# Kernel tuning notes

Measured on AMD Instinct MI355X. Metric: run time of the kernel, lower is better.

The kernel has to match this reference:

```python
import jax, jax.numpy as jnp
import numpy as np

NUM_CLASSES = 21
ALPHA = 1.0
NEG_POS_RATIO = 3.0
NEG_FOR_HARD = 100.0
B, N = 128, 8732


def setup_inputs() -> dict:
    key = jax.random.key(0)
    k1, k2, k3, k4, k5 = jax.random.split(key, 5)
    loc_pred = jax.random.normal(k1, (B, N, 4), jnp.float32)
    conf_pred = jax.random.normal(k2, (B, N, NUM_CLASSES), jnp.float32)
    # y_true = [loc_targets(4) | one-hot class(NUM_CLASSES) | pos_indicator(1)]
    loc_t = jax.random.normal(k3, (B, N, 4), jnp.float32)
    pos = (jax.random.uniform(k4, (B, N)) < 0.02).astype(jnp.float32)
    labels = jax.random.randint(k5, (B, N), 1, NUM_CLASSES)
    labels = jnp.where(pos > 0, labels, 0)  # negatives -> background class 0
    onehot = jax.nn.one_hot(labels, NUM_CLASSES, dtype=jnp.float32)
    y_true = jnp.concatenate([loc_t, onehot, pos[..., None]], axis=-1)
    return {"y_true": y_true, "loc_pred": loc_pred, "conf_pred": conf_pred}


def reference(y_true, loc_pred, conf_pred):
    num_boxes = y_true.shape[1]
    # conf part of y_pred is softmaxed before the loss (as in the torch code)
    conf = jax.nn.softmax(conf_pred, axis=-1)                    # (B, N, C)
    # cross-entropy with clamp(1e-7) + log, summed over classes
    conf_loss = -jnp.sum(y_true[:, :, 4:-1] * jnp.log(jnp.clip(conf, 1e-7, None)), axis=-1)  # (B, N)
    # smooth-L1 on the 4 loc coords
    d = y_true[:, :, :4] - loc_pred
    ad = jnp.abs(d)
    loc_loss = jnp.sum(jnp.where(ad < 1.0, 0.5 * d * d, ad - 0.5), axis=-1)  # (B, N)

    pos = y_true[:, :, -1]                                       # (B, N)
    pos_loc_loss = jnp.sum(loc_loss * pos, axis=1)               # (B,)
    pos_conf_loss = jnp.sum(conf_loss * pos, axis=1)             # (B,)

    num_pos = jnp.sum(pos, axis=-1)                              # (B,)
    num_neg = jnp.minimum(NEG_POS_RATIO * num_pos, num_boxes - num_pos)
    has_pos = jnp.sum((num_pos > 0).astype(jnp.float32)) > 0
    num_neg_batch = jnp.where(has_pos, jnp.sum(num_neg), jnp.float32(NEG_FOR_HARD))
    k_neg = jnp.floor(num_neg_batch)  # matches int() truncation in torch

    # hard-negative mining: max non-background confidence on negative anchors
    # confs_start=5, confs_end=4+NUM_CLASSES -> softmax classes 1..NUM_CLASSES-1
    max_confs = ((1.0 - pos) * jnp.sum(conf[:, :, 1:NUM_CLASSES], axis=2)).reshape(-1)  # (B*N,)
    order = jnp.argsort(-max_confs)                              # descending, static shape
    sorted_conf_loss = conf_loss.reshape(-1)[order]
    ranks = jnp.arange(max_confs.shape[0], dtype=jnp.float32)
    neg_conf_loss = jnp.sum(jnp.where(ranks < k_neg, sorted_conf_loss, 0.0))

    num_pos_c = jnp.where(num_pos != 0, num_pos, jnp.ones_like(num_pos))
    total = jnp.sum(pos_conf_loss) + neg_conf_loss + ALPHA * jnp.sum(pos_loc_loss)
    return total / jnp.sum(num_pos_c)
```

## Files before the change

### kernel.cpp

```cpp
#include <hip/hip_runtime.h>

#define BATCH 128
#define NBOX 8732
#define NC 21
#define M (BATCH * NBOX)
#define EBLK 2048
#define SUBB 16
#define CHUNK 546
#define NREP 32
#define CLIP_MAX 16.118095651f

struct Ctl {
  float pos_conf_sum, pos_loc_sum, s_gt, denom;
  unsigned int k_rem, d1, d2, pad;
};

#define OFF_NPP 1024
#define OFF_PCP (OFF_NPP + 8192)
#define OFF_PLP (OFF_PCP + 8192)
#define OFF_REP 32768
#define REPSZ   (NREP * 2048 * 4)
#define OFF_MC  (OFF_REP + 6 * REPSZ)
#define OFF_CL  (OFF_MC + M * 4)
#define ZERO_BYTES OFF_MC

__device__ __forceinline__ unsigned long long mckey(float mc) {
  unsigned long long K = (unsigned long long)((double)mc * 8589934592.0);
  return (K > 0x1FFFFFFFFull) ? 0x1FFFFFFFFull : K;
}

__global__ __launch_bounds__(256) void k_elem(
    const float* __restrict__ yt, const float* __restrict__ lp,
    const float* __restrict__ cp, float* __restrict__ MC,
    float* __restrict__ CL, float* __restrict__ np_part,
    float* __restrict__ pc_part, float* __restrict__ pl_part,
    unsigned int* __restrict__ rep1c, float* __restrict__ rep1s) {
  __shared__ unsigned int hc[2048];
  __shared__ float hs[2048];
  __shared__ float sred[12];
  const int tid = threadIdx.x;
  const int bid = blockIdx.x;
  for (int i = tid; i < 2048; i += 256) { hc[i] = 0u; hs[i] = 0.f; }
  __syncthreads();

  const int batch = bid >> 4;
  const int sub = bid & 15;
  const int base = batch * NBOX + sub * CHUNK;
  const int cnt = (sub == SUBB - 1) ? (NBOX - (SUBB - 1) * CHUNK) : CHUNK;

  float tpc = 0.f, tpl = 0.f, tnp = 0.f;
  for (int i = tid; i < cnt; i += 256) {
    const int e = base + i;
    const float* crow = cp + (size_t)e * NC;
    float cv[NC];
#pragma unroll
    for (int j = 0; j < NC; ++j) cv[j] = crow[j];
    const float2* y2 = (const float2*)(yt + (size_t)e * 26);
    float2 yw[13];
#pragma unroll
    for (int j = 0; j < 13; ++j) yw[j] = y2[j];
    const float4 lv = ((const float4*)lp)[e];
    const float pos = yw[12].y;

    const float d0 = yw[0].x - lv.x, d1 = yw[0].y - lv.y;
    const float d2 = yw[1].x - lv.z, d3 = yw[1].y - lv.w;
    const float a0 = fabsf(d0), a1 = fabsf(d1), a2 = fabsf(d2), a3 = fabsf(d3);
    float ll = ((a0 < 1.f) ? 0.5f * d0 * d0 : a0 - 0.5f)
             + ((a1 < 1.f) ? 0.5f * d1 * d1 : a1 - 0.5f)
             + ((a2 < 1.f) ? 0.5f * d2 * d2 : a2 - 0.5f)
             + ((a3 < 1.f) ? 0.5f * d3 * d3 : a3 - 0.5f);

    float mx = cv[0];
#pragma unroll
    for (int j = 1; j < NC; ++j) mx = fmaxf(mx, cv[j]);
    float plogit = 0.f;
#pragma unroll
    for (int j = 0; j < NC; ++j) {
      const int w = 4 + j;
      const float oh = (w & 1) ? yw[w >> 1].y : yw[w >> 1].x;
      plogit = fmaf(oh, cv[j], plogit);
    }
    float ssum = 0.f, e0 = 0.f;
#pragma unroll
    for (int j = 0; j < NC; ++j) {
      const float ee = __expf(cv[j] - mx);
      ssum += ee;
      if (j == 0) e0 = ee;
    }
    const float cl = fminf(mx + __logf(ssum) - plogit, CLIP_MAX);
    const float mc = (1.f - pos) * ((ssum - e0) / ssum);

    MC[e] = mc;
    CL[e] = cl;
    const unsigned int b1 = (unsigned int)(mckey(mc) >> 22);
    atomicAdd(&hc[b1], 1u);
    atomicAdd(&hs[b1], cl);
    tpc += pos * cl;
    tpl += pos * ll;
    tnp += pos;
  }

#pragma unroll
  for (int off = 32; off > 0; off >>= 1) {
    tpc += __shfl_down(tpc, off);
    tpl += __shfl_down(tpl, off);
    tnp += __shfl_down(tnp, off);
  }
  if ((tid & 63) == 0) {
    const int w = tid >> 6;
    sred[w] = tpc; sred[4 + w] = tpl; sred[8 + w] = tnp;
  }
  __syncthreads();
  if (tid == 0) {
    pc_part[bid] = sred[0] + sred[1] + sred[2] + sred[3];
    pl_part[bid] = sred[4] + sred[5] + sred[6] + sred[7];
    np_part[bid] = sred[8] + sred[9] + sred[10] + sred[11];
  }
  unsigned int* rc = rep1c + (bid & (NREP - 1)) * 2048;
  float* rs = rep1s + (bid & (NREP - 1)) * 2048;
  for (int i = tid; i < 2048; i += 256)
    if (hc[i]) { atomicAdd(&rc[i], hc[i]); atomicAdd(&rs[i], hs[i]); }
}

template <int LEVEL>
__global__ __launch_bounds__(256) void k_hist(
    const float* __restrict__ MC, const float* __restrict__ CL,
    unsigned int* __restrict__ repc, float* __restrict__ reps,
    const Ctl* __restrict__ ctl) {
  __shared__ unsigned int hc[2048];
  __shared__ float hs[2048];
  for (int i = threadIdx.x; i < 2048; i += 256) { hc[i] = 0u; hs[i] = 0.f; }
  __syncthreads();
  const unsigned int dd = (LEVEL == 2) ? ctl->d1 : ((ctl->d1 << 11) | ctl->d2);
  const float4* M4 = (const float4*)MC;
  const int n4 = M / 4;
  const int stride = gridDim.x * 256;
  for (int i = blockIdx.x * 256 + threadIdx.x; i < n4; i += stride) {
    const float4 m = M4[i];
    const float mv[4] = {m.x, m.y, m.z, m.w};
#pragma unroll
    for (int q = 0; q < 4; ++q) {
      const unsigned long long K = mckey(mv[q]);
      bool match; unsigned int bin;
      if (LEVEL == 2) { match = (unsigned int)(K >> 22) == dd; bin = (unsigned int)(K >> 11) & 2047u; }
      else            { match = (unsigned int)(K >> 11) == dd; bin = (unsigned int)K & 2047u; }
      if (match) {
        const float cl = CL[4 * i + q];
        atomicAdd(&hc[bin], 1u);
        atomicAdd(&hs[bin], cl);
      }
    }
  }
  __syncthreads();
  unsigned int* rc = repc + (blockIdx.x & (NREP - 1)) * 2048;
  float* rs = reps + (blockIdx.x & (NREP - 1)) * 2048;
  for (int i = threadIdx.x; i < 2048; i += 256)
    if (hc[i]) { atomicAdd(&rc[i], hc[i]); atomicAdd(&rs[i], hs[i]); }
}

template <int LEVEL>
__global__ __launch_bounds__(1024) void k_scan(
    const unsigned int* __restrict__ repc, const float* __restrict__ reps,
    const float* __restrict__ np_part, const float* __restrict__ pc_part,
    const float* __restrict__ pl_part, Ctl* __restrict__ ctl,
    float* __restrict__ out) {
  __shared__ unsigned int s[2048];
  __shared__ float sf[2048];
  __shared__ float red[16], rn[16], rh[16], rc[16], ra[16], rb[16];
  __shared__ unsigned int kk;
  __shared__ int win;
  const int tid = threadIdx.x;

  unsigned int c0 = 0, c1 = 0;
  float f0 = 0.f, f1 = 0.f;
  for (int r = 0; r < NREP; ++r) {
    c0 += repc[r * 2048 + tid];
    c1 += repc[r * 2048 + tid + 1024];
    f0 += reps[r * 2048 + tid];
    f1 += reps[r * 2048 + tid + 1024];
  }
  s[tid] = c0; s[tid + 1024] = c1;
  sf[tid] = f0; sf[tid + 1024] = f1;

  if (LEVEL == 1) {
    float np = 0.f;
    if (tid < BATCH)
      for (int j = 0; j < SUBB; ++j) np += np_part[tid * SUBB + j];
    float nn  = fminf(3.0f * np, (float)NBOX - np);
    float hp  = (np > 0.f) ? 1.f : 0.f;
    float npc = (tid < BATCH) ? ((np != 0.f) ? np : 1.f) : 0.f;
    float a = pc_part[tid] + pc_part[tid + 1024];
    float b = pl_part[tid] + pl_part[tid + 1024];
#pragma unroll
    for (int off = 32; off > 0; off >>= 1) {
      nn += __shfl_down(nn, off);   hp += __shfl_down(hp, off);
      npc += __shfl_down(npc, off); a += __shfl_down(a, off);
      b += __shfl_down(b, off);
    }
    const int w = tid >> 6;
    if ((tid & 63) == 0) { rn[w] = nn; rh[w] = hp; rc[w] = npc; ra[w] = a; rb[w] = b; }
    __syncthreads();
    if (tid == 0) {
      float tn = 0.f, th = 0.f, tc = 0.f, ta = 0.f, tb = 0.f;
      for (int i = 0; i < 16; ++i) { tn += rn[i]; th += rh[i]; tc += rc[i]; ta += ra[i]; tb += rb[i]; }
      ctl->denom = tc;
      ctl->pos_conf_sum = ta;
      ctl->pos_loc_sum = tb;
      kk = (unsigned int)floorf((th > 0.f) ? tn : 100.0f);
    }
  } else {
    if (tid == 0) kk = ctl->k_rem;
  }
  if (tid == 0) win = -1;
  __syncthreads();

  const unsigned int krem = kk;
  if (krem != 0) {
    for (int off = 1; off < 2048; off <<= 1) {
      const unsigned int v0 = (tid + off < 2048) ? s[tid + off] : 0u;
      const unsigned int v1 = (tid + 1024 + off < 2048) ? s[tid + 1024 + off] : 0u;
      __syncthreads();
      s[tid] += v0;
      s[tid + 1024] += v1;
      __syncthreads();
    }
#pragma unroll
    for (int t = 0; t < 2; ++t) {
      const int i = tid + t * 1024;
      const unsigned int si = s[i];
      const unsigned int sn = (i < 2047) ? s[i + 1] : 0u;
      if (si >= krem && sn < krem) win = i;
    }
    __syncthreads();
    const int b = win;
    float acc = 0.f;
    if (b >= 0) {
      if (tid > b) acc += sf[tid];
      if (tid + 1024 > b) acc += sf[tid + 1024];
    }
#pragma unroll
    for (int off = 32; off > 0; off >>= 1) acc += __shfl_down(acc, off);
    if ((tid & 63) == 0) red[tid >> 6] = acc;
    __syncthreads();
    if (tid == 0 && b >= 0) {
      float tot = 0.f;
      for (int i = 0; i < 16; ++i) tot += red[i];
      const unsigned int above = (b < 2047) ? s[b + 1] : 0u;
      const unsigned int krem2 = krem - above;
      if (LEVEL < 3) {
        ctl->s_gt += tot;
        ctl->k_rem = krem2;
        if (LEVEL == 1) ctl->d1 = (unsigned int)b;
        else            ctl->d2 = (unsigned int)b;
      } else {
        const unsigned int neq = s[b] - above;
        const float tie = (neq > 0) ? sf[b] * ((float)krem2 / (float)neq) : 0.f;
        const float neg = ctl->s_gt + tot + tie;
        out[0] = (ctl->pos_conf_sum + neg + ctl->pos_loc_sum) / ctl->denom;
      }
    }
  } else if (LEVEL == 3 && tid == 0) {
    out[0] = (ctl->pos_conf_sum + ctl->s_gt + ctl->pos_loc_sum) / ctl->denom;
  }
}

extern "C" void kernel_launch(void* const* d_in, const int* in_sizes, int n_in,
                              void* d_out, int out_size, void* d_ws, size_t ws_size,
                              hipStream_t stream) {
  const float* yt = (const float*)d_in[0];
  const float* lp = (const float*)d_in[1];
  const float* cp = (const float*)d_in[2];
  float* out = (float*)d_out;

  char* ws = (char*)d_ws;
  Ctl* ctl = (Ctl*)ws;
  float* np_part = (float*)(ws + OFF_NPP);
  float* pc_part = (float*)(ws + OFF_PCP);
  float* pl_part = (float*)(ws + OFF_PLP);
  unsigned int* rep1c = (unsigned int*)(ws + OFF_REP);
  float*        rep1s = (float*)(ws + OFF_REP + 1 * REPSZ);
  unsigned int* rep2c = (unsigned int*)(ws + OFF_REP + 2 * REPSZ);
  float*        rep2s = (float*)(ws + OFF_REP + 3 * REPSZ);
  unsigned int* rep3c = (unsigned int*)(ws + OFF_REP + 4 * REPSZ);
  float*        rep3s = (float*)(ws + OFF_REP + 5 * REPSZ);
  float* MC = (float*)(ws + OFF_MC);
  float* CL = (float*)(ws + OFF_CL);

  hipMemsetAsync(ws, 0, ZERO_BYTES, stream);
  k_elem<<<EBLK, 256, 0, stream>>>(yt, lp, cp, MC, CL, np_part, pc_part, pl_part,
                                   rep1c, rep1s);
  k_scan<1><<<1, 1024, 0, stream>>>(rep1c, rep1s, np_part, pc_part, pl_part, ctl, out);
  k_hist<2><<<1024, 256, 0, stream>>>(MC, CL, rep2c, rep2s, ctl);
  k_scan<2><<<1, 1024, 0, stream>>>(rep2c, rep2s, np_part, pc_part, pl_part, ctl, out);
  k_hist<3><<<1024, 256, 0, stream>>>(MC, CL, rep3c, rep3s, ctl);
  k_scan<3><<<1, 1024, 0, stream>>>(rep3c, rep3s, np_part, pc_part, pl_part, ctl, out);
}
```

Before: 289.7 us.

## Process each anchor row with a 32-lane group for coalesced loads; shrink replica histograms

The element kernel now assigns one anchor row to a 32-lane sub-group. Each lane loads one class logit, one y_true entry and one loc coordinate, and max, sum-exp, picked logit and smooth-L1 are combined with shuffle reductions. Before, one thread read a whole 21/26-float row, which gave strided, uncoalesced global loads. The level-2 and level-3 histogram replicas drop from 32 to 8, which shrinks the memset and the scan reads. The per-row work now costs many more shuffles and leaves lanes idle (11 of 32 unused for logits), and there are more global atomic collisions on fewer replicas.

```diff
diff --git a/kernel.cpp b/kernel.cpp
--- a/kernel.cpp
+++ b/kernel.cpp
@@ -7,7 +7,8 @@
 #define EBLK 2048
 #define SUBB 16
 #define CHUNK 546
-#define NREP 32
+#define NREP1 32
+#define NREP2 8
 #define CLIP_MAX 16.118095651f
 
 struct Ctl {
@@ -15,14 +16,21 @@
   unsigned int k_rem, d1, d2, pad;
 };
 
-#define OFF_NPP 1024
+#define OFF_REP 1024
+#define R1SZ    (NREP1 * 2048 * 4)
+#define R23SZ   (NREP2 * 2048 * 4)
+#define OFF_R1C (OFF_REP)
+#define OFF_R1S (OFF_R1C + R1SZ)
+#define OFF_R2C (OFF_R1S + R1SZ)
+#define OFF_R2S (OFF_R2C + R23SZ)
+#define OFF_R3C (OFF_R2S + R23SZ)
+#define OFF_R3S (OFF_R3C + R23SZ)
+#define OFF_NPP (OFF_R3S + R23SZ)
 #define OFF_PCP (OFF_NPP + 8192)
 #define OFF_PLP (OFF_PCP + 8192)
-#define OFF_REP 32768
-#define REPSZ   (NREP * 2048 * 4)
-#define OFF_MC  (OFF_REP + 6 * REPSZ)
+#define OFF_MC  (OFF_PLP + 8192)
 #define OFF_CL  (OFF_MC + M * 4)
-#define ZERO_BYTES OFF_MC
+#define ZERO_BYTES OFF_NPP
 
 __device__ __forceinline__ unsigned long long mckey(float mc) {
   unsigned long long K = (unsigned long long)((double)mc * 8589934592.0);
@@ -47,57 +55,54 @@
   const int sub = bid & 15;
   const int base = batch * NBOX + sub * CHUNK;
   const int cnt = (sub == SUBB - 1) ? (NBOX - (SUBB - 1) * CHUNK) : CHUNK;
+  const int g = tid >> 5;
+  const int j = tid & 31;
 
   float tpc = 0.f, tpl = 0.f, tnp = 0.f;
-  for (int i = tid; i < cnt; i += 256) {
-    const int e = base + i;
-    const float* crow = cp + (size_t)e * NC;
-    float cv[NC];
-#pragma unroll
-    for (int j = 0; j < NC; ++j) cv[j] = crow[j];
-    const float2* y2 = (const float2*)(yt + (size_t)e * 26);
-    float2 yw[13];
-#pragma unroll
-    for (int j = 0; j < 13; ++j) yw[j] = y2[j];
-    const float4 lv = ((const float4*)lp)[e];
-    const float pos = yw[12].y;
-
-    const float d0 = yw[0].x - lv.x, d1 = yw[0].y - lv.y;
-    const float d2 = yw[1].x - lv.z, d3 = yw[1].y - lv.w;
-    const float a0 = fabsf(d0), a1 = fabsf(d1), a2 = fabsf(d2), a3 = fabsf(d3);
-    float ll = ((a0 < 1.f) ? 0.5f * d0 * d0 : a0 - 0.5f)
-             + ((a1 < 1.f) ? 0.5f * d1 * d1 : a1 - 0.5f)
-             + ((a2 < 1.f) ? 0.5f * d2 * d2 : a2 - 0.5f)
-             + ((a3 < 1.f) ? 0.5f * d3 * d3 : a3 - 0.5f);
-
-    float mx = cv[0];
-#pragma unroll
-    for (int j = 1; j < NC; ++j) mx = fmaxf(mx, cv[j]);
-    float plogit = 0.f;
-#pragma unroll
-    for (int j = 0; j < NC; ++j) {
-      const int w = 4 + j;
-      const float oh = (w & 1) ? yw[w >> 1].y : yw[w >> 1].x;
-      plogit = fmaf(oh, cv[j], plogit);
-    }
-    float ssum = 0.f, e0 = 0.f;
-#pragma unroll
-    for (int j = 0; j < NC; ++j) {
-      const float ee = __expf(cv[j] - mx);
-      ssum += ee;
-      if (j == 0) e0 = ee;
-    }
-    const float cl = fminf(mx + __logf(ssum) - plogit, CLIP_MAX);
+  for (int i = g; i < cnt; i += 8) {
+    const int r = base + i;
+    float cv = -1e30f, yw = 0.f, lvj = 0.f;
+    if (j < NC) cv = cp[(size_t)r * NC + j];
+    if (j < 26) yw = yt[(size_t)r * 26 + j];
+    if (j < 4)  lvj = lp[(size_t)r * 4 + j];
+    const float pos = __shfl(yw, 25, 32);
+    const float oh  = __shfl(yw, j + 4, 32);
+
+    float mx = cv;
+    mx = fmaxf(mx, __shfl_xor(mx, 1, 32));
+    mx = fmaxf(mx, __shfl_xor(mx, 2, 32));
+    mx = fmaxf(mx, __shfl_xor(mx, 4, 32));
+    mx = fmaxf(mx, __shfl_xor(mx, 8, 32));
+    mx = fmaxf(mx, __shfl_xor(mx, 16, 32));
+
+    float ee = 0.f, pt = 0.f, sl = 0.f;
+    if (j < NC) { ee = __expf(cv - mx); pt = oh * cv; }
+    if (j < 4) {
+      const float d = yw - lvj, ad = fabsf(d);
+      sl = (ad < 1.f) ? 0.5f * d * d : ad - 0.5f;
+    }
+    const float e0 = __shfl(ee, 0, 32);
+    float ssum = ee, plog = pt, ll = sl;
+#pragma unroll
+    for (int m = 1; m < 32; m <<= 1) {
+      ssum += __shfl_xor(ssum, m, 32);
+      plog += __shfl_xor(plog, m, 32);
+      ll   += __shfl_xor(ll, m, 32);
+    }
+
+    const float cl = fminf(mx + __logf(ssum) - plog, CLIP_MAX);
     const float mc = (1.f - pos) * ((ssum - e0) / ssum);
 
-    MC[e] = mc;
-    CL[e] = cl;
-    const unsigned int b1 = (unsigned int)(mckey(mc) >> 22);
-    atomicAdd(&hc[b1], 1u);
-    atomicAdd(&hs[b1], cl);
-    tpc += pos * cl;
-    tpl += pos * ll;
-    tnp += pos;
+    if (j == 0) {
+      MC[r] = mc;
+      CL[r] = cl;
+      const unsigned int b1 = (unsigned int)(mckey(mc) >> 22);
+      atomicAdd(&hc[b1], 1u);
+      atomicAdd(&hs[b1], cl);
+      tpc += pos * cl;
+      tpl += pos * ll;
+      tnp += pos;
+    }
   }
 
 #pragma unroll
@@ -116,8 +121,8 @@
     pl_part[bid] = sred[4] + sred[5] + sred[6] + sred[7];
     np_part[bid] = sred[8] + sred[9] + sred[10] + sred[11];
   }
-  unsigned int* rc = rep1c + (bid & (NREP - 1)) * 2048;
-  float* rs = rep1s + (bid & (NREP - 1)) * 2048;
+  unsigned int* rc = rep1c + (bid & (NREP1 - 1)) * 2048;
+  float* rs = rep1s + (bid & (NREP1 - 1)) * 2048;
   for (int i = tid; i < 2048; i += 256)
     if (hc[i]) { atomicAdd(&rc[i], hc[i]); atomicAdd(&rs[i], hs[i]); }
 }
@@ -152,13 +157,13 @@
     }
   }
   __syncthreads();
-  unsigned int* rc = repc + (blockIdx.x & (NREP - 1)) * 2048;
-  float* rs = reps + (blockIdx.x & (NREP - 1)) * 2048;
+  unsigned int* rc = repc + (blockIdx.x & (NREP2 - 1)) * 2048;
+  float* rs = reps + (blockIdx.x & (NREP2 - 1)) * 2048;
   for (int i = threadIdx.x; i < 2048; i += 256)
     if (hc[i]) { atomicAdd(&rc[i], hc[i]); atomicAdd(&rs[i], hs[i]); }
 }
 
-template <int LEVEL>
+template <int LEVEL, int NREP>
 __global__ __launch_bounds__(1024) void k_scan(
     const unsigned int* __restrict__ repc, const float* __restrict__ reps,
     const float* __restrict__ np_part, const float* __restrict__ pc_part,
@@ -185,7 +190,7 @@
   if (LEVEL == 1) {
     float np = 0.f;
     if (tid < BATCH)
-      for (int j = 0; j < SUBB; ++j) np += np_part[tid * SUBB + j];
+      for (int jj = 0; jj < SUBB; ++jj) np += np_part[tid * SUBB + jj];
     float nn  = fminf(3.0f * np, (float)NBOX - np);
     float hp  = (np > 0.f) ? 1.f : 0.f;
     float npc = (tid < BATCH) ? ((np != 0.f) ? np : 1.f) : 0.f;
@@ -274,24 +279,24 @@
 
   char* ws = (char*)d_ws;
   Ctl* ctl = (Ctl*)ws;
+  unsigned int* rep1c = (unsigned int*)(ws + OFF_R1C);
+  float*        rep1s = (float*)(ws + OFF_R1S);
+  unsigned int* rep2c = (unsigned int*)(ws + OFF_R2C);
+  float*        rep2s = (float*)(ws + OFF_R2S);
+  unsigned int* rep3c = (unsigned int*)(ws + OFF_R3C);
+  float*        rep3s = (float*)(ws + OFF_R3S);
   float* np_part = (float*)(ws + OFF_NPP);
   float* pc_part = (float*)(ws + OFF_PCP);
   float* pl_part = (float*)(ws + OFF_PLP);
-  unsigned int* rep1c = (unsigned int*)(ws + OFF_REP);
-  float*        rep1s = (float*)(ws + OFF_REP + 1 * REPSZ);
-  unsigned int* rep2c = (unsigned int*)(ws + OFF_REP + 2 * REPSZ);
-  float*        rep2s = (float*)(ws + OFF_REP + 3 * REPSZ);
-  unsigned int* rep3c = (unsigned int*)(ws + OFF_REP + 4 * REPSZ);
-  float*        rep3s = (float*)(ws + OFF_REP + 5 * REPSZ);
   float* MC = (float*)(ws + OFF_MC);
   float* CL = (float*)(ws + OFF_CL);
 
   hipMemsetAsync(ws, 0, ZERO_BYTES, stream);
   k_elem<<<EBLK, 256, 0, stream>>>(yt, lp, cp, MC, CL, np_part, pc_part, pl_part,
                                    rep1c, rep1s);
-  k_scan<1><<<1, 1024, 0, stream>>>(rep1c, rep1s, np_part, pc_part, pl_part, ctl, out);
+  k_scan<1, NREP1><<<1, 1024, 0, stream>>>(rep1c, rep1s, np_part, pc_part, pl_part, ctl, out);
   k_hist<2><<<1024, 256, 0, stream>>>(MC, CL, rep2c, rep2s, ctl);
-  k_scan<2><<<1, 1024, 0, stream>>>(rep2c, rep2s, np_part, pc_part, pl_part, ctl, out);
+  k_scan<2, NREP2><<<1, 1024, 0, stream>>>(rep2c, rep2s, np_part, pc_part, pl_part, ctl, out);
   k_hist<3><<<1024, 256, 0, stream>>>(MC, CL, rep3c, rep3s, ctl);
-  k_scan<3><<<1, 1024, 0, stream>>>(rep3c, rep3s, np_part, pc_part, pl_part, ctl, out);
-}
+  k_scan<3, NREP2><<<1, 1024, 0, stream>>>(rep3c, rep3s, np_part, pc_part, pl_part, ctl, out);
+}
```

New measurement: 363.7 us. 25.5% more time.
